# Kernel tuning notes

Hardware: AMD Instinct MI355X
Metric: run time of the kernel (lower is better)

Reference implementation:

```python
import jax, jax.numpy as jnp
import numpy as np

B = 32
HIST, C, H, W = 10, 11, 15, 20
D, NH, NL = 256, 4, 4
HD = D // NH
OUT, ADIM = 256, 20
L = HIST * H * W + 1  # 3001 tokens incl. cls
VIS = HIST * C * H * W  # 33000


def layernorm(x, g, b, eps=1e-5):
    m = jnp.mean(x, axis=-1, keepdims=True)
    v = jnp.mean((x - m) ** 2, axis=-1, keepdims=True)
    return (x - m) * jax.lax.rsqrt(v + eps) * g + b


def rope_1d(x):
    # x: [B, NH, L, HD]
    l, hd = x.shape[2], x.shape[3]
    t = jnp.arange(l, dtype=x.dtype)
    freqs = 10000.0 ** (-jnp.arange(0, hd, 2, dtype=x.dtype) / hd)
    emb = t[:, None] * freqs[None, :]            # [L, HD/2]
    emb = jnp.concatenate([emb, emb], axis=-1)   # [L, HD]
    cos = jnp.cos(emb)[None, None]
    sin = jnp.sin(emb)[None, None]
    x1, x2 = x[..., : hd // 2], x[..., hd // 2 :]
    rot = jnp.concatenate([-x2, x1], axis=-1)
    return x * cos + rot * sin


def lightning_attn(x, qw, kw, vw, ow, gq, bq, gk, bk):
    b, l, _ = x.shape
    q = layernorm(x @ qw, gq, bq)
    k = layernorm(x @ kw, gk, bk)
    v = x @ vw
    split = lambda a: a.reshape(b, l, NH, HD).transpose(0, 2, 1, 3)  # [B,NH,L,HD]
    q, k, v = split(q), split(k), split(v)
    q = jax.nn.silu(rope_1d(q))
    k = jax.nn.silu(rope_1d(k))
    kv = jnp.einsum('bhld,bhle->bhde', k, v)            # O(L) kv accumulation
    out = jnp.einsum('bhld,bhde->bhle', q, kv)
    out = out / jnp.sqrt(jnp.asarray(HD, x.dtype))
    out = out.transpose(0, 2, 1, 3).reshape(b, l, D)
    return out @ ow


def forward(obs_stack, proj_w, proj_b, cls_token, qw, kw, vw, ow, gq, bq, gk, bk,
            n1g, n1b, n2g, n2b, w1, b1, w2, b2, fng, fnb, out_w, out_b):
    b = obs_stack.shape[0]
    obs_feat = obs_stack[:, :VIS]
    action_feat = obs_stack[:, VIS:]
    vision = obs_feat.reshape(b, HIST, C, H, W).transpose(0, 1, 3, 4, 2)  # [B,T,H,W,C]
    x = vision @ proj_w + proj_b                                          # [B,T,H,W,D]
    x = x.reshape(b, -1, D)
    cls = jnp.broadcast_to(cls_token, (b, 1, D))
    x = jnp.concatenate([cls, x], axis=1)                                 # [B,L,D]
    for i in range(NL):
        h = lightning_attn(layernorm(x, n1g[i], n1b[i]), qw[i], kw[i], vw[i], ow[i],
                           gq[i], bq[i], gk[i], bk[i])
        x = x + h
        y = layernorm(x, n2g[i], n2b[i])
        y = jax.nn.gelu(y @ w1[i] + b1[i], approximate=False) @ w2[i] + b2[i]
        x = x + y
    x = layernorm(x, fng, fnb)
    cls_out = x[:, 0, :]
    final = jnp.concatenate([cls_out, action_feat], axis=1)
    return final @ out_w + out_b


def setup_inputs() -> dict:
    key = jax.random.key(0)
    ks = jax.random.split(key, 16)
    s = 0.02
    n = lambda k, shp: jax.random.normal(k, shp, dtype=jnp.float32) * s
    inp = {
        'obs_stack': jax.random.normal(ks[0], (B, VIS + ADIM), dtype=jnp.float32),
        'proj_w': n(ks[1], (C, D)),
        'proj_b': jnp.zeros((D,), jnp.float32),
        'cls_token': jax.random.normal(ks[2], (1, 1, D), dtype=jnp.float32),
        'qw': n(ks[3], (NL, D, D)),
        'kw': n(ks[4], (NL, D, D)),
        'vw': n(ks[5], (NL, D, D)),
        'ow': n(ks[6], (NL, D, D)),
        'gq': jnp.ones((NL, D), jnp.float32),
        'bq': jnp.zeros((NL, D), jnp.float32),
        'gk': jnp.ones((NL, D), jnp.float32),
        'bk': jnp.zeros((NL, D), jnp.float32),
        'n1g': jnp.ones((NL, D), jnp.float32),
        'n1b': jnp.zeros((NL, D), jnp.float32),
        'n2g': jnp.ones((NL, D), jnp.float32),
        'n2b': jnp.zeros((NL, D), jnp.float32),
        'w1': n(ks[7], (NL, D, 4 * D)),
        'b1': jnp.zeros((NL, 4 * D), jnp.float32),
        'w2': n(ks[8], (NL, 4 * D, D)),
        'b2': jnp.zeros((NL, D), jnp.float32),
        'fng': jnp.ones((D,), jnp.float32),
        'fnb': jnp.zeros((D,), jnp.float32),
        'out_w': n(ks[9], (D + ADIM, OUT)),
        'out_b': jnp.zeros((OUT,), jnp.float32),
    }
    return inp


def reference(obs_stack, proj_w, proj_b, cls_token, qw, kw, vw, ow, gq, bq, gk, bk,
              n1g, n1b, n2g, n2b, w1, b1, w2, b2, fng, fnb, out_w, out_b):
    return forward(obs_stack, proj_w, proj_b, cls_token, qw, kw, vw, ow, gq, bq, gk, bk,
                   n1g, n1b, n2g, n2b, w1, b1, w2, b2, fng, fnb, out_w, out_b)
```

## Files before the change

### kernel.cpp

```cpp
#include <hip/hip_runtime.h>
#include <math.h>

typedef unsigned short u16;
typedef __attribute__((ext_vector_type(8))) short short8;
typedef __attribute__((ext_vector_type(4))) short short4v;
typedef __attribute__((ext_vector_type(4))) float f32x4;

constexpr int B_    = 32;
constexpr int HIST_ = 10, C_ = 11, H_ = 15, W_ = 20;
constexpr int D_    = 256, NH_ = 4, NL_ = 4, HD_ = 64;
constexpr int OUT_  = 256, ADIM_ = 20;
constexpr int L_    = HIST_*H_*W_ + 1;
constexpr int VIS_  = HIST_*C_*H_*W_;
constexpr int NTOK  = B_*L_;
constexpr int OBSROW = VIS_ + ADIM_;
constexpr int PADR  = 128;

__device__ __forceinline__ float bf2f(u16 u) {
    return __uint_as_float(((unsigned)u) << 16);
}
__device__ __forceinline__ u16 f2bf(float f) {
    unsigned u = __float_as_uint(f);
    u = u + 0x7FFFu + ((u >> 16) & 1u);
    return (u16)(u >> 16);
}
__device__ __forceinline__ f32x4 mfma16(short8 a, short8 b, f32x4 c) {
    return __builtin_amdgcn_mfma_f32_16x16x32_bf16(a, b, c, 0, 0, 0);
}
__device__ __forceinline__ void gload16(const u16* gsrc, u16* ldsdst) {
    __builtin_amdgcn_global_load_lds(
        (const __attribute__((address_space(1))) unsigned int*)gsrc,
        (__attribute__((address_space(3))) unsigned int*)ldsdst,
        16, 0, 0);
}
__device__ __forceinline__ float gelu_fast(float v) {
    float t2 = 1.5957691216f*(v + 0.044715f*v*v*v);
    return v / (1.f + __expf(-t2));
}

__global__ void zero_kernel(float* __restrict__ p, int n) {
    int i = blockIdx.x*256 + threadIdx.x;
    if (i < n) p[i] = 0.f;
}

__global__ void wcvt_kernel(const float* __restrict__ src, u16* __restrict__ dst,
                            int Nn, int Kk, int dstLS, int dstOff) {
    int idx = blockIdx.x*256 + threadIdx.x;
    int tot = NL_*Nn*Kk;
    if (idx >= tot) return;
    int l = idx / (Nn*Kk);
    int rem = idx % (Nn*Kk);
    int n = rem / Kk, k = rem % Kk;
    dst[(size_t)l*dstLS + (size_t)(dstOff+n)*Kk + k] = f2bf(src[(size_t)l*Kk*Nn + (size_t)k*Nn + n]);
}

__global__ void rope_table_kernel(float* __restrict__ tab) {
    int idx = blockIdx.x*256 + threadIdx.x;
    if (idx >= L_*32) return;
    int t = idx >> 5, i = idx & 31;
    float freq = powf(10000.f, -2.f*(float)i/(float)HD_);
    float ang = (float)t * freq;
    tab[idx*2]   = cosf(ang);
    tab[idx*2+1] = sinf(ang);
}

__global__ __launch_bounds__(256) void proj_kernel(const float* __restrict__ obs,
        const float* __restrict__ pw, const float* __restrict__ pb,
        const float* __restrict__ cls, float* __restrict__ x) {
    int wave = threadIdx.x >> 6, lane = threadIdx.x & 63;
    int n = blockIdx.x*4 + wave;
    if (n >= NTOK) return;
    int b = n / L_, l = n % L_;
    float4 acc;
    if (l == 0) {
        acc = ((const float4*)cls)[lane];
    } else {
        int t = l - 1;
        int hist = t / (H_*W_);
        int rem  = t % (H_*W_);
        float vv = 0.f;
        if (lane < C_) vv = obs[(size_t)b*OBSROW + hist*(C_*H_*W_) + lane*(H_*W_) + rem];
        acc = ((const float4*)pb)[lane];
        #pragma unroll
        for (int c = 0; c < C_; ++c) {
            float vc = __shfl(vv, c);
            float4 w4 = ((const float4*)(pw + c*D_))[lane];
            acc.x += vc*w4.x; acc.y += vc*w4.y; acc.z += vc*w4.z; acc.w += vc*w4.w;
        }
    }
    ((float4*)(x + (size_t)n*D_))[lane] = acc;
}

__global__ __launch_bounds__(256) void ln_f2b_kernel(const float* __restrict__ in,
        const float* __restrict__ g, const float* __restrict__ bt,
        u16* __restrict__ out, int ntok) {
    int wave = threadIdx.x >> 6, lane = threadIdx.x & 63;
    int n = blockIdx.x*4 + wave;
    if (n >= ntok) return;
    float4 v = ((const float4*)(in + (size_t)n*D_))[lane];
    float s  = v.x + v.y + v.z + v.w;
    float sq = v.x*v.x + v.y*v.y + v.z*v.z + v.w*v.w;
    #pragma unroll
    for (int off = 32; off; off >>= 1) { s += __shfl_xor(s, off); sq += __shfl_xor(sq, off); }
    float mean = s * (1.f/D_);
    float var  = sq * (1.f/D_) - mean*mean;
    float r = rsqrtf(var + 1e-5f);
    float4 gg = ((const float4*)g)[lane];
    float4 bb = ((const float4*)bt)[lane];
    short4v o;
    o.x = (short)f2bf((v.x-mean)*r*gg.x + bb.x);
    o.y = (short)f2bf((v.y-mean)*r*gg.y + bb.y);
    o.z = (short)f2bf((v.z-mean)*r*gg.z + bb.z);
    o.w = (short)f2bf((v.w-mean)*r*gg.w + bb.w);
    *(short4v*)(out + (size_t)n*D_ + lane*4) = o;
}

__global__ __launch_bounds__(256) void lnres_kernel(float* __restrict__ x,
        u16* __restrict__ dx, const float* __restrict__ g, const float* __restrict__ bt,
        int ntok) {
    int wave = threadIdx.x >> 6, lane = threadIdx.x & 63;
    int n = blockIdx.x*4 + wave;
    if (n >= ntok) return;
    float4 v = ((const float4*)(x + (size_t)n*D_))[lane];
    short4v d = *(const short4v*)(dx + (size_t)n*D_ + lane*4);
    v.x += bf2f((u16)d.x); v.y += bf2f((u16)d.y);
    v.z += bf2f((u16)d.z); v.w += bf2f((u16)d.w);
    ((float4*)(x + (size_t)n*D_))[lane] = v;
    float s  = v.x + v.y + v.z + v.w;
    float sq = v.x*v.x + v.y*v.y + v.z*v.z + v.w*v.w;
    #pragma unroll
    for (int off = 32; off; off >>= 1) { s += __shfl_xor(s, off); sq += __shfl_xor(sq, off); }
    float mean = s * (1.f/D_);
    float var  = sq * (1.f/D_) - mean*mean;
    float r = rsqrtf(var + 1e-5f);
    float4 gg = ((const float4*)g)[lane];
    float4 bb = ((const float4*)bt)[lane];
    short4v o;
    o.x = (short)f2bf((v.x-mean)*r*gg.x + bb.x);
    o.y = (short)f2bf((v.y-mean)*r*gg.y + bb.y);
    o.z = (short)f2bf((v.z-mean)*r*gg.z + bb.z);
    o.w = (short)f2bf((v.w-mean)*r*gg.w + bb.w);
    *(short4v*)(dx + (size_t)n*D_ + lane*4) = o;
}

__global__ __launch_bounds__(256) void lnrope_kernel(u16* __restrict__ qk,
        const float* __restrict__ gq, const float* __restrict__ bq,
        const float* __restrict__ gk, const float* __restrict__ bk,
        const float* __restrict__ tab, int ntok, int ld) {
    u16* q = qk + blockIdx.y*256;
    const float* g  = blockIdx.y ? gk : gq;
    const float* bt = blockIdx.y ? bk : bq;
    int wave = threadIdx.x >> 6, lane = threadIdx.x & 63;
    int n = blockIdx.x*4 + wave;
    if (n >= ntok) return;
    int l = n % L_;
    short4v raw = *(const short4v*)(q + (size_t)n*ld + lane*4);
    float v0 = bf2f((u16)raw.x), v1 = bf2f((u16)raw.y), v2 = bf2f((u16)raw.z), v3 = bf2f((u16)raw.w);
    float s  = v0+v1+v2+v3;
    float sq = v0*v0+v1*v1+v2*v2+v3*v3;
    #pragma unroll
    for (int off = 32; off; off >>= 1) { s += __shfl_xor(s, off); sq += __shfl_xor(sq, off); }
    float mean = s * (1.f/D_);
    float var  = sq * (1.f/D_) - mean*mean;
    float r = rsqrtf(var + 1e-5f);
    float4 gg = ((const float4*)g)[lane];
    float4 bb = ((const float4*)bt)[lane];
    float o0 = (v0-mean)*r*gg.x + bb.x;
    float o1 = (v1-mean)*r*gg.y + bb.y;
    float o2 = (v2-mean)*r*gg.z + bb.z;
    float o3 = (v3-mean)*r*gg.w + bb.w;
    float p0 = __shfl_xor(o0, 8), p1 = __shfl_xor(o1, 8);
    float p2 = __shfl_xor(o2, 8), p3 = __shfl_xor(o3, 8);
    bool first = (lane & 15) < 8;
    const float4* tp = (const float4*)(tab + ((size_t)l*32 + (lane&7)*4)*2);
    float4 t01 = tp[0], t23 = tp[1];
    float r0 = first ? o0*t01.x - p0*t01.y : o0*t01.x + p0*t01.y;
    float r1 = first ? o1*t01.z - p1*t01.w : o1*t01.z + p1*t01.w;
    float r2 = first ? o2*t23.x - p2*t23.y : o2*t23.x + p2*t23.y;
    float r3 = first ? o3*t23.z - p3*t23.w : o3*t23.z + p3*t23.w;
    r0 = r0 / (1.f + expf(-r0));
    r1 = r1 / (1.f + expf(-r1));
    r2 = r2 / (1.f + expf(-r2));
    r3 = r3 / (1.f + expf(-r3));
    short4v o;
    o.x = (short)f2bf(r0); o.y = (short)f2bf(r1);
    o.z = (short)f2bf(r2); o.w = (short)f2bf(r3);
    *(short4v*)(q + (size_t)n*ld + lane*4) = o;
}

template<int EPI, bool PB>
__global__ __launch_bounds__(256) void gemm_bf16(const u16* __restrict__ A, int lda,
        const u16* __restrict__ Wt, const float* __restrict__ bias,
        u16* __restrict__ Cb, float* __restrict__ Xres, int M, int N, int K, int ldc) {
    __shared__ u16 As[2*128*32];
    __shared__ u16 Bs[2*128*32];
    const int gx = gridDim.x;
    int n = blockIdx.y * gx + blockIdx.x;
    const int nwg = gx * gridDim.y;
    if ((nwg & 7) == 0) n = (n & 7) * (nwg >> 3) + (n >> 3);
    const int bx = n % gx, by = n / gx;
    const int row0 = by*128, col0 = bx*128;

    size_t zrow = 0;
    if (PB) {
        int z = blockIdx.z;
        A  += (size_t)z * M * lda;
        Wt += (size_t)z * N * K;
        zrow = (size_t)z * M;
    }

    const int tid = threadIdx.x;
    const int wid = tid >> 6, lane = tid & 63;
    const int wr = wid >> 1, wc = wid & 1;

    f32x4 acc[4][4];
    #pragma unroll
    for (int i = 0; i < 4; ++i)
        #pragma unroll
        for (int j = 0; j < 4; ++j) {
            f32x4 z; z.x = 0.f; z.y = 0.f; z.z = 0.f; z.w = 0.f;
            acc[i][j] = z;
        }

    const int r0s = wid*32 + (lane>>2);
    const int r1s = r0s + 16;
    const int s0 = ((lane&3) - (r0s>>1)) & 3;
    const int s1 = ((lane&3) - (r1s>>1)) & 3;
    const u16* a0p = A  + (size_t)(row0 + r0s)*lda + s0*8;
    const u16* a1p = A  + (size_t)(row0 + r1s)*lda + s1*8;
    const u16* b0p = Wt + (size_t)(col0 + r0s)*K + s0*8;
    const u16* b1p = Wt + (size_t)(col0 + r1s)*K + s1*8;
    u16* lA0 = As + (wid*2+0)*512;
    u16* lA1 = As + (wid*2+1)*512;
    u16* lB0 = Bs + (wid*2+0)*512;
    u16* lB1 = Bs + (wid*2+1)*512;

    const int kg = lane >> 4, li = lane & 15;
    int aoff[4], boff[4];
    #pragma unroll
    for (int mi = 0; mi < 4; ++mi) {
        int row = wr*64 + mi*16 + li;
        aoff[mi] = row*32 + ((kg + (row>>1)) & 3)*8;
    }
    #pragma unroll
    for (int ni = 0; ni < 4; ++ni) {
        int row = wc*64 + ni*16 + li;
        boff[ni] = row*32 + ((kg + (row>>1)) & 3)*8;
    }

    auto stage = [&](int k0) {
        #pragma unroll
        for (int t = 0; t < 2; ++t) {
            const int ko = k0 + t*32;
            const int lo = t*4096;
            gload16(a0p + ko, lA0 + lo); gload16(a1p + ko, lA1 + lo);
            gload16(b0p + ko, lB0 + lo); gload16(b1p + ko, lB1 + lo);
        }
    };

    stage(0);
    const int nk2 = K >> 6;
    for (int ks = 0; ks < nk2; ++ks) {
        __syncthreads();
        short8 af[2][4], bfr[2][4];
        #pragma unroll
        for (int t = 0; t < 2; ++t) {
            #pragma unroll
            for (int mi = 0; mi < 4; ++mi) af[t][mi] = *(const short8*)(As + t*4096 + aoff[mi]);
            #pragma unroll
            for (int ni = 0; ni < 4; ++ni) bfr[t][ni] = *(const short8*)(Bs + t*4096 + boff[ni]);
        }
        __syncthreads();
        if (ks + 1 < nk2) stage((ks + 1) << 6);
        #pragma unroll
        for (int t = 0; t < 2; ++t)
            #pragma unroll
            for (int mi = 0; mi < 4; ++mi)
                #pragma unroll
                for (int ni = 0; ni < 4; ++ni)
                    acc[mi][ni] = mfma16(af[t][mi], bfr[t][ni], acc[mi][ni]);
    }

    #pragma unroll
    for (int mi = 0; mi < 4; ++mi) {
        int rbase = row0 + wr*64 + mi*16 + kg*4;
        #pragma unroll
        for (int ni = 0; ni < 4; ++ni) {
            int col = col0 + wc*64 + ni*16 + li;
            #pragma unroll
            for (int r = 0; r < 4; ++r) {
                int row = rbase + r;
                if (row >= M) continue;
                float v = acc[mi][ni][r];
                if (EPI == 1 || EPI == 3 || EPI == 4) v += bias[col];
                if (EPI == 1) v = gelu_fast(v);
                if (EPI == 0 || EPI == 1 || EPI == 4)
                    Cb[(zrow + row)*(size_t)ldc + col] = f2bf(v);
                else
                    Xres[(zrow + row)*(size_t)ldc + col] += v;
            }
        }
    }
}

template<int EPI, bool PB>
__global__ __launch_bounds__(512) void gemm_wide(const u16* __restrict__ A, int lda,
        const u16* __restrict__ Wt, const float* __restrict__ bias,
        u16* __restrict__ Cb, int M, int N, int K, int ldc) {
    __shared__ u16 As[2*4096];
    __shared__ u16 Bs[2*8192];
    const int gx = gridDim.x;
    int n = blockIdx.y * gx + blockIdx.x;
    const int nwg = gx * gridDim.y;
    if ((nwg & 7) == 0) n = (n & 7) * (nwg >> 3) + (n >> 3);
    const int bx = n % gx, by = n / gx;
    const int row0 = by*128, col0 = bx*256;

    size_t zrow = 0;
    if (PB) {
        int z = blockIdx.z;
        A  += (size_t)z * M * lda;
        Wt += (size_t)z * N * K;
        zrow = (size_t)z * M;
    }

    const int tid = threadIdx.x;
    const int wid = tid >> 6, lane = tid & 63;
    const int kg = lane >> 4, li = lane & 15;

    f32x4 acc[16];
    #pragma unroll
    for (int i = 0; i < 16; ++i) { f32x4 z; z.x=0.f; z.y=0.f; z.z=0.f; z.w=0.f; acc[i]=z; }

    const int ra = wid*16 + (lane>>2);
    const int sa = ((lane&3) - (ra>>1)) & 3;
    const u16* agp = A + (size_t)(row0 + ra)*lda + sa*8;
    const int lAo = wid*512;
    const int rb0 = (wid*2+0)*16 + (lane>>2);
    const int rb1 = (wid*2+1)*16 + (lane>>2);
    const int sb0 = ((lane&3) - (rb0>>1)) & 3;
    const int sb1 = ((lane&3) - (rb1>>1)) & 3;
    const u16* bgp0 = Wt + (size_t)(col0 + rb0)*K + sb0*8;
    const u16* bgp1 = Wt + (size_t)(col0 + rb1)*K + sb1*8;
    const int lB0o = (wid*2+0)*512;
    const int lB1o = (wid*2+1)*512;

    const int arow = wid*16 + li;
    const int aoff = arow*32 + ((kg + (arow>>1)) & 3)*8;
    int boff[16];
    #pragma unroll
    for (int ni = 0; ni < 16; ++ni) {
        int row = ni*16 + li;
        boff[ni] = row*32 + ((kg + (row>>1)) & 3)*8;
    }

    auto stage = [&](int k0) {
        #pragma unroll
        for (int t = 0; t < 2; ++t) {
            const int ko = k0 + t*32;
            gload16(agp  + ko, As + t*4096 + lAo);
            gload16(bgp0 + ko, Bs + t*8192 + lB0o);
            gload16(bgp1 + ko, Bs + t*8192 + lB1o);
        }
    };

    stage(0);
    const int nk2 = K >> 6;
    for (int ks = 0; ks < nk2; ++ks) {
        __syncthreads();
        short8 af0 = *(const short8*)(As + aoff);
        short8 b0[8], b1[8];
        #pragma unroll
        for (int ni = 0; ni < 8; ++ni) b0[ni] = *(const short8*)(Bs + boff[ni]);
        #pragma unroll
        for (int ni = 0; ni < 8; ++ni) acc[ni] = mfma16(af0, b0[ni], acc[ni]);
        #pragma unroll
        for (int ni = 0; ni < 8; ++ni) b1[ni] = *(const short8*)(Bs + boff[8+ni]);
        #pragma unroll
        for (int ni = 0; ni < 8; ++ni) acc[8+ni] = mfma16(af0, b1[ni], acc[8+ni]);
        short8 af1 = *(const short8*)(As + 4096 + aoff);
        #pragma unroll
        for (int ni = 0; ni < 8; ++ni) b0[ni] = *(const short8*)(Bs + 8192 + boff[ni]);
        #pragma unroll
        for (int ni = 0; ni < 8; ++ni) b1[ni] = *(const short8*)(Bs + 8192 + boff[8+ni]);
        __syncthreads();
        if (ks + 1 < nk2) stage((ks + 1) << 6);
        #pragma unroll
        for (int ni = 0; ni < 8; ++ni) acc[ni]   = mfma16(af1, b0[ni], acc[ni]);
        #pragma unroll
        for (int ni = 0; ni < 8; ++ni) acc[8+ni] = mfma16(af1, b1[ni], acc[8+ni]);
    }

    #pragma unroll
    for (int r = 0; r < 4; ++r) {
        const int row = row0 + wid*16 + kg*4 + r;
        if (row >= M) continue;
        #pragma unroll
        for (int ni = 0; ni < 16; ++ni) {
            int col = col0 + ni*16 + li;
            float v = acc[ni][r];
            if (EPI == 1) { v += bias[col]; v = gelu_fast(v); }
            Cb[(zrow + row)*(size_t)ldc + col] = f2bf(v);
        }
    }
}

constexpr int KV_LSPLIT = 4;
constexpr int KV_PART   = 768;
__global__ __launch_bounds__(256) void kv_mfma_kernel(const u16* __restrict__ Kt,
        const u16* __restrict__ Vt, float* __restrict__ kvf, int ld) {
    __shared__ u16 kT[64][34];
    __shared__ u16 vT[64][34];
    const int bh = blockIdx.x;
    const int b = bh >> 2, h = bh & 3;
    const int tid = threadIdx.x;
    const int wid = tid >> 6, lane = tid & 63;
    const int kg = lane >> 4, li = lane & 15;
    const int wm = (wid >> 1)*32, wn = (wid & 1)*32;
    const int sl = tid >> 3;
    const int sd = (tid & 7) * 8;
    const u16* kbase = Kt + ((size_t)b*L_)*ld + h*HD_ + sd;
    const u16* vbase = Vt + ((size_t)b*L_)*ld + h*HD_ + sd;

    f32x4 acc[2][2];
    #pragma unroll
    for (int i = 0; i < 2; ++i)
        #pragma unroll
        for (int j = 0; j < 2; ++j) {
            f32x4 z; z.x=0.f; z.y=0.f; z.z=0.f; z.w=0.f; acc[i][j] = z;
        }

    const int l0p = blockIdx.y * KV_PART;
    for (int t = 0; t < KV_PART/32; ++t) {
        int gl = l0p + t*32 + sl;
        short8 kk = {0,0,0,0,0,0,0,0}, vv = {0,0,0,0,0,0,0,0};
        if (gl < L_) {
            kk = *(const short8*)(kbase + (size_t)gl*ld);
            vv = *(const short8*)(vbase + (size_t)gl*ld);
        }
        __syncthreads();
        #pragma unroll
        for (int j = 0; j < 8; ++j) {
            kT[sd+j][sl] = (u16)kk[j];
            vT[sd+j][sl] = (u16)vv[j];
        }
        __syncthreads();
        short8 a0, a1, b0, b1;
        {
            uint* d0 = (uint*)&a0; const uint* p0 = (const uint*)&kT[wm + li][kg*8];
            uint* d1 = (uint*)&a1; const uint* p1 = (const uint*)&kT[wm + 16 + li][kg*8];
            uint* d2 = (uint*)&b0; const uint* p2 = (const uint*)&vT[wn + li][kg*8];
            uint* d3 = (uint*)&b1; const uint* p3 = (const uint*)&vT[wn + 16 + li][kg*8];
            #pragma unroll
            for (int j = 0; j < 4; ++j) { d0[j]=p0[j]; d1[j]=p1[j]; d2[j]=p2[j]; d3[j]=p3[j]; }
        }
        acc[0][0] = mfma16(a0, b0, acc[0][0]);
        acc[0][1] = mfma16(a0, b1, acc[0][1]);
        acc[1][0] = mfma16(a1, b0, acc[1][0]);
        acc[1][1] = mfma16(a1, b1, acc[1][1]);
    }
    float* base = kvf + (size_t)bh*4096;
    #pragma unroll
    for (int mi = 0; mi < 2; ++mi)
        #pragma unroll
        for (int ni = 0; ni < 2; ++ni)
            #pragma unroll
            for (int r = 0; r < 4; ++r)
                atomicAdd(base + (wm + mi*16 + kg*4 + r)*64 + wn + ni*16 + li,
                          acc[mi][ni][r]);
}

__global__ __launch_bounds__(256) void m2_kernel(const float* __restrict__ kvf,
        const float* __restrict__ ow, u16* __restrict__ m2t) {
    __shared__ float kvs[64][64];
    const int bh = blockIdx.x;
    const int b = bh >> 2, h = bh & 3;
    const int tid = threadIdx.x;
    #pragma unroll
    for (int p = 0; p < 16; ++p)
        ((float*)kvs)[p*256 + tid] = kvf[(size_t)bh*4096 + p*256 + tid];
    __syncthreads();
    float acc[64];
    #pragma unroll
    for (int d = 0; d < 64; ++d) acc[d] = 0.f;
    for (int e = 0; e < 64; ++e) {
        float w = ow[(size_t)(h*64 + e)*256 + tid];
        #pragma unroll
        for (int d = 0; d < 64; ++d) acc[d] += kvs[d][e] * w;
    }
    u16* dst = m2t + ((size_t)b*256 + tid)*256 + h*64;
    #pragma unroll
    for (int d = 0; d < 64; ++d) dst[d] = f2bf(acc[d]*0.125f);
}

__global__ void head_kernel(const float* __restrict__ x, const float* __restrict__ obs,
                            const float* __restrict__ fng, const float* __restrict__ fnb,
                            const float* __restrict__ ow, const float* __restrict__ ob,
                            float* __restrict__ out) {
    __shared__ float row[D_ + ADIM_];
    __shared__ float red[8];
    int b = blockIdx.x, tid = threadIdx.x;
    float v = x[((size_t)b*L_)*D_ + tid];
    float s = v, sq = v*v;
    #pragma unroll
    for (int off = 32; off; off >>= 1) { s += __shfl_xor(s, off); sq += __shfl_xor(sq, off); }
    int wave = tid >> 6, lane = tid & 63;
    if (lane == 0) { red[wave] = s; red[4+wave] = sq; }
    __syncthreads();
    s  = red[0]+red[1]+red[2]+red[3];
    sq = red[4]+red[5]+red[6]+red[7];
    float mean = s*(1.f/D_), var = sq*(1.f/D_) - mean*mean;
    float r = rsqrtf(var + 1e-5f);
    row[tid] = (v-mean)*r*fng[tid] + fnb[tid];
    if (tid < ADIM_) row[D_+tid] = obs[(size_t)b*OBSROW + VIS_ + tid];
    __syncthreads();
    float acc = ob[tid];
    for (int j = 0; j < D_+ADIM_; ++j) acc += row[j]*ow[j*OUT_ + tid];
    out[(size_t)b*OUT_ + tid] = acc;
}

extern "C" void kernel_launch(void* const* d_in, const int* in_sizes, int n_in,
                              void* d_out, int out_size, void* d_ws, size_t ws_size,
                              hipStream_t stream) {
    const float* obs   = (const float*)d_in[0];
    const float* pw    = (const float*)d_in[1];
    const float* pb    = (const float*)d_in[2];
    const float* cls   = (const float*)d_in[3];
    const float* qw    = (const float*)d_in[4];
    const float* kw    = (const float*)d_in[5];
    const float* vw    = (const float*)d_in[6];
    const float* oww   = (const float*)d_in[7];
    const float* gq    = (const float*)d_in[8];
    const float* bq    = (const float*)d_in[9];
    const float* gk    = (const float*)d_in[10];
    const float* bk    = (const float*)d_in[11];
    const float* n1g   = (const float*)d_in[12];
    const float* n1b   = (const float*)d_in[13];
    const float* n2g   = (const float*)d_in[14];
    const float* n2b   = (const float*)d_in[15];
    const float* w1    = (const float*)d_in[16];
    const float* b1    = (const float*)d_in[17];
    const float* w2    = (const float*)d_in[18];
    const float* b2    = (const float*)d_in[19];
    const float* fng   = (const float*)d_in[20];
    const float* fnb   = (const float*)d_in[21];
    const float* outw  = (const float*)d_in[22];
    const float* outb  = (const float*)d_in[23];

    float* x = (float*)d_ws;
    u16* qkvT = (u16*)(x + (size_t)NTOK*D_);
    u16* w1T  = qkvT + (size_t)NL_*768*256;
    u16* w2T  = w1T  + (size_t)NL_*262144;
    float* tab = (float*)(w2T + (size_t)NL_*262144);
    u16* bufs = (u16*)(tab + (size_t)L_*32*2);

    size_t fixedB = (size_t)((char*)bufs - (char*)d_ws);
    auto needed = [&](int nb) -> size_t {
        size_t t = (size_t)nb * L_;
        return fixedB + (t*256 + (size_t)PADR*256)*2 + (t*1024 + (size_t)PADR*1024)*2
               + (size_t)nb*65536*2 + (size_t)nb*NH_*4096*4;
    };
    int nbc = 32;
    while (nbc > 1 && needed(nbc) > ws_size) nbc >>= 1;
    const int nch = B_ / nbc;
    const int RCn = nbc * L_;

    u16* Xn   = bufs;
    u16* QKVc = Xn + (size_t)RCn*256 + (size_t)PADR*256;
    u16* Hc   = QKVc;
    u16* M2T  = QKVc + (size_t)RCn*1024 + (size_t)PADR*1024;
    float* kvf = (float*)(M2T + (size_t)nbc*65536);

    wcvt_kernel<<<(NL_*65536 + 255)/256, 256, 0, stream>>>(qw,  qkvT, 256, 256, 768*256, 0);
    wcvt_kernel<<<(NL_*65536 + 255)/256, 256, 0, stream>>>(kw,  qkvT, 256, 256, 768*256, 256);
    wcvt_kernel<<<(NL_*65536 + 255)/256, 256, 0, stream>>>(vw,  qkvT, 256, 256, 768*256, 512);
    wcvt_kernel<<<(NL_*262144 + 255)/256, 256, 0, stream>>>(w1, w1T, 1024, 256, 262144, 0);
    wcvt_kernel<<<(NL_*262144 + 255)/256, 256, 0, stream>>>(w2, w2T, 256, 1024, 262144, 0);
    rope_table_kernel<<<(L_*32 + 255)/256, 256, 0, stream>>>(tab);
    proj_kernel<<<(NTOK + 3)/4, 256, 0, stream>>>(obs, pw, pb, cls, x);

    const int gy  = (RCn + 127)/128;
    const int lnb = (RCn + 3)/4;
    const int nbh = nbc*NH_;

    for (int c = 0; c < nch; ++c) {
        float* xc = x + (size_t)c*RCn*D_;
        ln_f2b_kernel<<<lnb, 256, 0, stream>>>(xc, n1g, n1b, Xn, RCn);

        for (int layer = 0; layer < NL_; ++layer) {
            const u16* qkvT_l = qkvT + (size_t)layer*768*256;
            const u16* w1T_l  = w1T  + (size_t)layer*262144;
            const u16* w2T_l  = w2T  + (size_t)layer*262144;
            const float* ow_l = oww + (size_t)layer*65536;
            const float* b1_l = b1 + (size_t)layer*1024;
            const float* b2_l = b2 + (size_t)layer*D_;

            gemm_wide<0,false><<<dim3(3, gy), 512, 0, stream>>>(Xn, 256, qkvT_l, nullptr, QKVc, RCn, 768, 256, 768);
            lnrope_kernel<<<dim3(lnb, 2), 256, 0, stream>>>(QKVc, gq + layer*D_, bq + layer*D_,
                                                            gk + layer*D_, bk + layer*D_, tab, RCn, 768);
            zero_kernel<<<(nbh*4096 + 255)/256, 256, 0, stream>>>(kvf, nbh*4096);
            kv_mfma_kernel<<<dim3(nbh, KV_LSPLIT), 256, 0, stream>>>(QKVc + 256, QKVc + 512, kvf, 768);
            m2_kernel<<<nbh, 256, 0, stream>>>(kvf, ow_l, M2T);
            gemm_bf16<0,true><<<dim3(2, 24, nbc), 256, 0, stream>>>(QKVc, 768, M2T, nullptr, Xn, nullptr, L_, 256, 256, 256);
            lnres_kernel<<<lnb, 256, 0, stream>>>(xc, Xn, n2g + layer*D_, n2b + layer*D_, RCn);
            gemm_wide<1,false><<<dim3(4, gy), 512, 0, stream>>>(Xn, 256, w1T_l, b1_l, Hc, RCn, 1024, 256, 1024);
            gemm_bf16<4,false><<<dim3(2, gy), 256, 0, stream>>>(Hc, 1024, w2T_l, b2_l, Xn, nullptr, RCn, 256, 1024, 256);
            const float* gN = (layer < NL_-1) ? (n1g + (layer+1)*D_) : fng;
            const float* bN = (layer < NL_-1) ? (n1b + (layer+1)*D_) : fnb;
            lnres_kernel<<<lnb, 256, 0, stream>>>(xc, Xn, gN, bN, RCn);
        }
    }

    head_kernel<<<B_, 256, 0, stream>>>(x, obs, fng, fnb, outw, outb, (float*)d_out);
}
```

Before: 2.488 ms.

## Compute only cls-token rows in the final layer's attention-out and MLP

The head reads only the cls token from the last layer output. For the final layer, the full-sequence attention-output GEMM, post-attention layernorm and the two MLP GEMMs are replaced by a single tail kernel that runs only on the cls row of each batch element. It uses scalar FMAs over the bf16 weights and updates x in place for that row. The other token rows of the final layer are left stale, which is valid because only the cls row is consumed. The unused residual epilogue branch in gemm_bf16 is also removed.

Result: faster. 2.262 ms (-9.1%).

```diff
diff --git a/kernel.cpp b/kernel.cpp
--- a/kernel.cpp
+++ b/kernel.cpp
@@ -292,12 +292,9 @@
                 int row = rbase + r;
                 if (row >= M) continue;
                 float v = acc[mi][ni][r];
-                if (EPI == 1 || EPI == 3 || EPI == 4) v += bias[col];
+                if (EPI == 1 || EPI == 4) v += bias[col];
                 if (EPI == 1) v = gelu_fast(v);
-                if (EPI == 0 || EPI == 1 || EPI == 4)
-                    Cb[(zrow + row)*(size_t)ldc + col] = f2bf(v);
-                else
-                    Xres[(zrow + row)*(size_t)ldc + col] += v;
+                Cb[(zrow + row)*(size_t)ldc + col] = f2bf(v);
             }
         }
     }
@@ -491,6 +488,69 @@
     u16* dst = m2t + ((size_t)b*256 + tid)*256 + h*64;
     #pragma unroll
     for (int d = 0; d < 64; ++d) dst[d] = f2bf(acc[d]*0.125f);
+}
+
+__global__ __launch_bounds__(256) void tail_kernel(const u16* __restrict__ Q, int ldq,
+        const u16* __restrict__ m2t, float* __restrict__ x,
+        const float* __restrict__ g2, const float* __restrict__ bt2,
+        const u16* __restrict__ w1T, const float* __restrict__ b1v,
+        const u16* __restrict__ w2T, const float* __restrict__ b2v) {
+    __shared__ float qrow[256];
+    __shared__ float y[256];
+    __shared__ float h[1024];
+    __shared__ float red[8];
+    const int bl = blockIdx.x;
+    const int tid = threadIdx.x;
+    const size_t row = (size_t)bl * L_;
+    qrow[tid] = bf2f(Q[row*(size_t)ldq + tid]);
+    __syncthreads();
+    const u16* mrow = m2t + ((size_t)bl*256 + tid)*256;
+    float acc = 0.f;
+    for (int d = 0; d < 256; d += 8) {
+        short8 w = *(const short8*)(mrow + d);
+        acc += qrow[d+0]*bf2f((u16)w[0]) + qrow[d+1]*bf2f((u16)w[1])
+             + qrow[d+2]*bf2f((u16)w[2]) + qrow[d+3]*bf2f((u16)w[3])
+             + qrow[d+4]*bf2f((u16)w[4]) + qrow[d+5]*bf2f((u16)w[5])
+             + qrow[d+6]*bf2f((u16)w[6]) + qrow[d+7]*bf2f((u16)w[7]);
+    }
+    float v = x[row*256 + tid] + acc;
+    float s = v, sq = v*v;
+    #pragma unroll
+    for (int off = 32; off; off >>= 1) { s += __shfl_xor(s, off); sq += __shfl_xor(sq, off); }
+    int wave = tid >> 6, lane = tid & 63;
+    if (lane == 0) { red[wave] = s; red[4+wave] = sq; }
+    __syncthreads();
+    s  = red[0]+red[1]+red[2]+red[3];
+    sq = red[4]+red[5]+red[6]+red[7];
+    float mean = s*(1.f/256.f), var = sq*(1.f/256.f) - mean*mean;
+    float rstd = rsqrtf(var + 1e-5f);
+    y[tid] = (v - mean)*rstd*g2[tid] + bt2[tid];
+    __syncthreads();
+    #pragma unroll
+    for (int jj = 0; jj < 4; ++jj) {
+        int j = tid*4 + jj;
+        const u16* wrow = w1T + (size_t)j*256;
+        float a = b1v[j];
+        for (int k = 0; k < 256; k += 8) {
+            short8 w = *(const short8*)(wrow + k);
+            a += y[k+0]*bf2f((u16)w[0]) + y[k+1]*bf2f((u16)w[1])
+               + y[k+2]*bf2f((u16)w[2]) + y[k+3]*bf2f((u16)w[3])
+               + y[k+4]*bf2f((u16)w[4]) + y[k+5]*bf2f((u16)w[5])
+               + y[k+6]*bf2f((u16)w[6]) + y[k+7]*bf2f((u16)w[7]);
+        }
+        h[j] = gelu_fast(a);
+    }
+    __syncthreads();
+    const u16* w2row = w2T + (size_t)tid*1024;
+    float a2 = b2v[tid];
+    for (int k = 0; k < 1024; k += 8) {
+        short8 w = *(const short8*)(w2row + k);
+        a2 += h[k+0]*bf2f((u16)w[0]) + h[k+1]*bf2f((u16)w[1])
+            + h[k+2]*bf2f((u16)w[2]) + h[k+3]*bf2f((u16)w[3])
+            + h[k+4]*bf2f((u16)w[4]) + h[k+5]*bf2f((u16)w[5])
+            + h[k+6]*bf2f((u16)w[6]) + h[k+7]*bf2f((u16)w[7]);
+    }
+    x[row*256 + tid] = v + a2;
 }
 
 __global__ void head_kernel(const float* __restrict__ x, const float* __restrict__ obs,
@@ -601,13 +661,18 @@
             zero_kernel<<<(nbh*4096 + 255)/256, 256, 0, stream>>>(kvf, nbh*4096);
             kv_mfma_kernel<<<dim3(nbh, KV_LSPLIT), 256, 0, stream>>>(QKVc + 256, QKVc + 512, kvf, 768);
             m2_kernel<<<nbh, 256, 0, stream>>>(kvf, ow_l, M2T);
-            gemm_bf16<0,true><<<dim3(2, 24, nbc), 256, 0, stream>>>(QKVc, 768, M2T, nullptr, Xn, nullptr, L_, 256, 256, 256);
-            lnres_kernel<<<lnb, 256, 0, stream>>>(xc, Xn, n2g + layer*D_, n2b + layer*D_, RCn);
-            gemm_wide<1,false><<<dim3(4, gy), 512, 0, stream>>>(Xn, 256, w1T_l, b1_l, Hc, RCn, 1024, 256, 1024);
-            gemm_bf16<4,false><<<dim3(2, gy), 256, 0, stream>>>(Hc, 1024, w2T_l, b2_l, Xn, nullptr, RCn, 256, 1024, 256);
-            const float* gN = (layer < NL_-1) ? (n1g + (layer+1)*D_) : fng;
-            const float* bN = (layer < NL_-1) ? (n1b + (layer+1)*D_) : fnb;
-            lnres_kernel<<<lnb, 256, 0, stream>>>(xc, Xn, gN, bN, RCn);
+
+            if (layer < NL_-1) {
+                gemm_bf16<0,true><<<dim3(2, 24, nbc), 256, 0, stream>>>(QKVc, 768, M2T, nullptr, Xn, nullptr, L_, 256, 256, 256);
+                lnres_kernel<<<lnb, 256, 0, stream>>>(xc, Xn, n2g + layer*D_, n2b + layer*D_, RCn);
+                gemm_wide<1,false><<<dim3(4, gy), 512, 0, stream>>>(Xn, 256, w1T_l, b1_l, Hc, RCn, 1024, 256, 1024);
+                gemm_bf16<4,false><<<dim3(2, gy), 256, 0, stream>>>(Hc, 1024, w2T_l, b2_l, Xn, nullptr, RCn, 256, 1024, 256);
+                lnres_kernel<<<lnb, 256, 0, stream>>>(xc, Xn, n1g + (layer+1)*D_, n1b + (layer+1)*D_, RCn);
+            } else {
+                tail_kernel<<<nbc, 256, 0, stream>>>(QKVc, 768, M2T, xc,
+                                                     n2g + layer*D_, n2b + layer*D_,
+                                                     w1T_l, b1_l, w2T_l, b2_l);
+            }
         }
     }
 
```
